# Kernel optimization log

Hardware: AMD Instinct MI355X
Metric: run time of the kernel (lower is better)

Reference implementation:

```python
import jax, jax.numpy as jnp
import numpy as np
import math

DIM = 512
BLOCK_NUM = 16
SEQ_LEN = 8192
BLOCK_LEN = SEQ_LEN // BLOCK_NUM  # 512 == DIM -> mask used as-is
BATCH = 4
LN_EPS = 1e-3  # keras LayerNormalization default epsilon


def setup_inputs() -> dict:
    key = jax.random.key(0)
    ks = jax.random.split(key, 5)
    inputs = jax.random.normal(ks[0], (BATCH, BLOCK_NUM, BLOCK_LEN, DIM), dtype=jnp.float32)
    # binary padding-style mask, values in {0,1}
    mask_array = jax.random.randint(ks[1], (BATCH, SEQ_LEN, DIM), 0, 2).astype(jnp.float32)
    scale = 1.0 / math.sqrt(DIM)
    dw1 = jax.random.normal(ks[2], (DIM, DIM), dtype=jnp.float32) * scale
    dw2 = jax.random.normal(ks[3], (DIM, DIM), dtype=jnp.float32) * scale
    dw3 = jax.random.normal(ks[4], (DIM, DIM), dtype=jnp.float32) * scale
    db1 = jnp.zeros((DIM,), dtype=jnp.float32)
    db2 = jnp.zeros((DIM,), dtype=jnp.float32)
    db3 = jnp.zeros((DIM,), dtype=jnp.float32)
    return {"inputs": inputs, "mask_array": mask_array,
            "dw1": dw1, "dw2": dw2, "dw3": dw3,
            "db1": db1, "db2": db2, "db3": db3}


def reference(inputs, mask_array, dw1, dw2, dw3, db1, db2, db3):
    # inputs: [B, block_num, block_len, dim]
    Q = jnp.matmul(inputs, dw1) + db1
    K = jnp.matmul(inputs, dw2) + db2
    V = jnpp_matmul = jnp.matmul(inputs, dw3) + db3
    V = jnp.matmul(inputs, dw3) + db3
    # block-local attention scores: [B, bn, bl, bl]
    scores = jnp.einsum('bnqd,bnkd->bnqk', Q, K) / math.sqrt(DIM)
    # mask: [B, seq_len, dim] -> [B, bn, bl, dim]; block_len == dim so no slice/tile
    m = mask_array.reshape(BATCH, BLOCK_NUM, BLOCK_LEN, DIM)
    scores = scores + (1.0 - m) * jnp.float32(-1e10)
    p = jax.nn.softmax(scores, axis=-1)
    out = jnp.einsum('bnqk,bnkd->bnqd', p, V) + inputs  # residual
    # LayerNorm(axis=-1), fresh keras layer: gamma=1, beta=0, eps=1e-3
    mean = jnp.mean(out, axis=-1, keepdims=True)
    var = jnp.mean(jnp.square(out - mean), axis=-1, keepdims=True)
    return (out - mean) / jnp.sqrt(var + LN_EPS)
```

## Files before the change

### kernel.cpp

```cpp
#include <hip/hip_runtime.h>

#define DIMK 512
#define NBLK 64
#define NTOK 32768

typedef short  short8 __attribute__((ext_vector_type(8)));
typedef float  f32x4  __attribute__((ext_vector_type(4)));
typedef unsigned short u16x8 __attribute__((ext_vector_type(8)));

__device__ __forceinline__ unsigned short f2bf(float f) {
  union { float f; unsigned u; } v; v.f = f;
  unsigned r = (v.u + 0x7FFFu + ((v.u >> 16) & 1u)) >> 16;
  return (unsigned short)r;
}
__device__ __forceinline__ float bf2f(unsigned short h) {
  return __uint_as_float(((unsigned)h) << 16);
}

__device__ __forceinline__ void gload_lds16(const unsigned short* g,
                                            unsigned short* l) {
  __builtin_amdgcn_global_load_lds(
      (const __attribute__((address_space(1))) unsigned int*)(g),
      (__attribute__((address_space(3))) unsigned int*)(l),
      16, 0, 0);
}

__global__ __launch_bounds__(256) void k_wt_prep(
    const float* __restrict__ dw1, const float* __restrict__ dw2,
    const float* __restrict__ dw3, unsigned short* __restrict__ Wt)
{
  const int idx = blockIdx.x * 256 + threadIdx.x;
  const int w = idx >> 18;
  const int r = idx & 262143;
  const int n = r >> 9, k = r & 511;
  const float* dw = (w == 0) ? dw1 : (w == 1) ? dw2 : dw3;
  Wt[(size_t)w * 262144 + (size_t)n * 512 + k] = f2bf(dw[(size_t)k * 512 + n]);
}

__global__ __launch_bounds__(256) void k_xconv(
    const float* __restrict__ X, unsigned short* __restrict__ Xb)
{
  const size_t i = ((size_t)blockIdx.x * 256 + threadIdx.x) * 8;
  const float4 a = *(const float4*)(X + i);
  const float4 b = *(const float4*)(X + i + 4);
  u16x8 o;
  o[0] = f2bf(a.x); o[1] = f2bf(a.y); o[2] = f2bf(a.z); o[3] = f2bf(a.w);
  o[4] = f2bf(b.x); o[5] = f2bf(b.y); o[6] = f2bf(b.z); o[7] = f2bf(b.w);
  *(u16x8*)(Xb + i) = o;
}

__global__ __launch_bounds__(256) void k_bitpack(
    const float* __restrict__ mask, unsigned char* __restrict__ bits)
{
  const size_t gid = (size_t)blockIdx.x * 256 + threadIdx.x;
  const size_t i = gid * 8;
  const float4 ma = *(const float4*)(mask + i);
  const float4 mb = *(const float4*)(mask + i + 4);
  unsigned v = 0;
  v |= (ma.x > 0.5f) << 0; v |= (ma.y > 0.5f) << 1;
  v |= (ma.z > 0.5f) << 2; v |= (ma.w > 0.5f) << 3;
  v |= (mb.x > 0.5f) << 4; v |= (mb.y > 0.5f) << 5;
  v |= (mb.z > 0.5f) << 6; v |= (mb.w > 0.5f) << 7;
  bits[gid] = (unsigned char)v;
}

__global__ __launch_bounds__(256, 2) void k_qkv(
    const unsigned short* __restrict__ Xb, const unsigned short* __restrict__ Wt,
    const float* __restrict__ db1, const float* __restrict__ db2,
    const float* __restrict__ db3,
    unsigned short* __restrict__ Qb, unsigned short* __restrict__ Kb,
    unsigned short* __restrict__ Vt)
{
  __shared__ __align__(16) unsigned short smem[128 * 136];
  unsigned short* As = smem;
  unsigned short* Bs = smem + 4096;

  const int id = blockIdx.x;
  const int x = id & 7, j = id >> 3;
  const int mtile = x * 32 + (j >> 2);
  const int nt = j & 3;
  const size_t m0 = (size_t)mtile * 128;
  const int n0 = nt * 128;

  const int tid = threadIdx.x, lane = tid & 63, wv = tid >> 6;
  const int quad = lane >> 4, l16 = lane & 15;
  const int rb = (wv >> 1) * 64, cb = (wv & 1) * 64;

  f32x4 acc[3][4][4];
#pragma unroll
  for (int w = 0; w < 3; ++w)
#pragma unroll
    for (int i = 0; i < 4; ++i)
#pragma unroll
      for (int jj = 0; jj < 4; ++jj) {
        f32x4 z = {0.f, 0.f, 0.f, 0.f}; acc[w][i][jj] = z;
      }

  const int ra0 = tid >> 2,          oa0 = (tid & 3) << 3;
  const int ra1 = (tid + 256) >> 2,  oa1 = ((tid + 256) & 3) << 3;
  const unsigned short* a0 = &Xb[(m0 + ra0) * (size_t)DIMK + oa0];
  const unsigned short* a1 = &Xb[(m0 + ra1) * (size_t)DIMK + oa1];

  for (int it = 0; it < 16; ++it) {
    const int k0 = it * 32;
    gload_lds16(a0 + k0, &As[tid * 8]);
    gload_lds16(a1 + k0, &As[(tid + 256) * 8]);
#pragma unroll
    for (int h = 0; h < 6; ++h) {
      const int c = tid + h * 256;
      const int w = c >> 9, cc = c & 511;
      const int r = cc >> 2, o = (cc & 3) << 3;
      gload_lds16(&Wt[(size_t)w * 262144 + (size_t)(n0 + r) * 512 + k0 + o],
                  &Bs[w * 4096 + cc * 8]);
    }
    __syncthreads();
    short8 af[4];
#pragma unroll
    for (int i = 0; i < 4; ++i)
      af[i] = *(const short8*)&As[(rb + i * 16 + l16) * 32 + quad * 8];
#pragma unroll
    for (int jj = 0; jj < 4; ++jj)
#pragma unroll
      for (int w = 0; w < 3; ++w) {
        const short8 bf =
            *(const short8*)&Bs[w * 4096 + (cb + jj * 16 + l16) * 32 + quad * 8];
#pragma unroll
        for (int i = 0; i < 4; ++i)
          acc[w][i][jj] = __builtin_amdgcn_mfma_f32_16x16x32_bf16(
              af[i], bf, acc[w][i][jj], 0, 0, 0);
      }
    __syncthreads();
  }

#pragma unroll
  for (int w = 0; w < 2; ++w) {
    const float* db = (w == 0) ? db1 : db2;
    unsigned short* Ob = (w == 0) ? Qb : Kb;
#pragma unroll
    for (int i = 0; i < 4; ++i)
#pragma unroll
      for (int jj = 0; jj < 4; ++jj)
#pragma unroll
        for (int r = 0; r < 4; ++r) {
          const size_t row = m0 + rb + i * 16 + quad * 4 + r;
          const int col = n0 + cb + jj * 16 + l16;
          Ob[row * (size_t)DIMK + col] = f2bf(acc[w][i][jj][r] + db[col]);
        }
  }
#pragma unroll
  for (int i = 0; i < 4; ++i)
#pragma unroll
    for (int jj = 0; jj < 4; ++jj) {
      const int cl = cb + jj * 16 + l16;
      const int t0 = rb + i * 16 + quad * 4;
      const float bv = db3[n0 + cl];
      ushort4 pk;
      pk.x = f2bf(acc[2][i][jj][0] + bv);
      pk.y = f2bf(acc[2][i][jj][1] + bv);
      pk.z = f2bf(acc[2][i][jj][2] + bv);
      pk.w = f2bf(acc[2][i][jj][3] + bv);
      *(ushort4*)&smem[cl * 136 + t0] = pk;
    }
  __syncthreads();
  const int blk = mtile >> 2;
  const int tokbase = (mtile & 3) * 128;
  unsigned short* Vblk = Vt + (size_t)blk * 262144;
#pragma unroll
  for (int h = 0; h < 8; ++h) {
    const int c = tid + h * 256;
    const int cl = c >> 4, toff = (c & 15) * 8;
    *(u16x8*)&Vblk[(size_t)(n0 + cl) * 512 + tokbase + toff] =
        *(const u16x8*)&smem[cl * 136 + toff];
  }
}

__global__ __launch_bounds__(256, 2) void k_attn_p(
    const unsigned short* __restrict__ Qb, const unsigned short* __restrict__ Kb,
    const unsigned long long* __restrict__ bits, unsigned short* __restrict__ Pb)
{
  __shared__ __align__(16) unsigned short As[64 * 32];
  __shared__ __align__(16) unsigned short Bs[512 * 32];
  __shared__ float red[4][64];
  const int tid = threadIdx.x, lane = tid & 63, wv = tid >> 6;
  const int quad = lane >> 4, l16 = lane & 15;
  const int blk = blockIdx.x & 63, mt = blockIdx.x >> 6;
  const size_t tb = (size_t)blk * 512;
  const size_t q0 = tb + (size_t)mt * 64;

  f32x4 acc[4][8];
#pragma unroll
  for (int i = 0; i < 4; ++i)
#pragma unroll
    for (int j = 0; j < 8; ++j) { f32x4 z = {0.f, 0.f, 0.f, 0.f}; acc[i][j] = z; }

  const int ra = tid >> 2, oa = (tid & 3) << 3;
  const unsigned short* ap = &Qb[(q0 + ra) * (size_t)DIMK + oa];
  const unsigned short* kp = &Kb[tb * (size_t)DIMK];

  for (int it = 0; it < 16; ++it) {
    const int k0 = it * 32;
    gload_lds16(ap + k0, &As[tid * 8]);
#pragma unroll
    for (int h = 0; h < 8; ++h) {
      const int c = tid + h * 256;
      const int r = c >> 2, o = (c & 3) << 3;
      gload_lds16(kp + (size_t)r * DIMK + k0 + o, &Bs[c * 8]);
    }
    __syncthreads();
    short8 af[4], bfv[8];
#pragma unroll
    for (int i = 0; i < 4; ++i)
      af[i] = *(const short8*)&As[(i * 16 + l16) * 32 + quad * 8];
#pragma unroll
    for (int j = 0; j < 8; ++j)
      bfv[j] = *(const short8*)&Bs[(wv * 128 + j * 16 + l16) * 32 + quad * 8];
#pragma unroll
    for (int i = 0; i < 4; ++i)
#pragma unroll
      for (int j = 0; j < 8; ++j)
        acc[i][j] = __builtin_amdgcn_mfma_f32_16x16x32_bf16(
            af[i], bfv[j], acc[i][j], 0, 0, 0);
    __syncthreads();
  }

  const float scale = 0.04419417382415922f;
  float rmax[4][4];
#pragma unroll
  for (int i = 0; i < 4; ++i)
#pragma unroll
    for (int r = 0; r < 4; ++r) rmax[i][r] = -3.0e38f;
#pragma unroll
  for (int i = 0; i < 4; ++i)
#pragma unroll
    for (int r = 0; r < 4; ++r) {
      const size_t tok = q0 + i * 16 + quad * 4 + r;
      const unsigned long long w0 = bits[tok * 8 + wv * 2];
      const unsigned long long w1 = bits[tok * 8 + wv * 2 + 1];
#pragma unroll
      for (int j = 0; j < 8; ++j) {
        const unsigned long long sel = (j < 4) ? w0 : w1;
        const float bias = ((sel >> (l16 + 16 * (j & 3))) & 1ull) ? 0.0f : -1e10f;
        const float v = acc[i][j][r] * scale + bias;
        acc[i][j][r] = v;
        rmax[i][r] = fmaxf(rmax[i][r], v);
      }
    }
#pragma unroll
  for (int i = 0; i < 4; ++i)
#pragma unroll
    for (int r = 0; r < 4; ++r)
      for (int d = 1; d < 16; d <<= 1)
        rmax[i][r] = fmaxf(rmax[i][r], __shfl_xor(rmax[i][r], d, 64));
  if (l16 == 0)
#pragma unroll
    for (int i = 0; i < 4; ++i)
#pragma unroll
      for (int r = 0; r < 4; ++r) red[wv][i * 16 + quad * 4 + r] = rmax[i][r];
  __syncthreads();
#pragma unroll
  for (int i = 0; i < 4; ++i)
#pragma unroll
    for (int r = 0; r < 4; ++r) {
      const int row = i * 16 + quad * 4 + r;
      rmax[i][r] = fmaxf(fmaxf(red[0][row], red[1][row]),
                         fmaxf(red[2][row], red[3][row]));
    }
  __syncthreads();
  float rsum[4][4];
#pragma unroll
  for (int i = 0; i < 4; ++i)
#pragma unroll
    for (int r = 0; r < 4; ++r) rsum[i][r] = 0.f;
#pragma unroll
  for (int i = 0; i < 4; ++i)
#pragma unroll
    for (int j = 0; j < 8; ++j)
#pragma unroll
      for (int r = 0; r < 4; ++r) {
        const float e = __expf(acc[i][j][r] - rmax[i][r]);
        acc[i][j][r] = e;
        rsum[i][r] += e;
      }
#pragma unroll
  for (int i = 0; i < 4; ++i)
#pragma unroll
    for (int r = 0; r < 4; ++r)
      for (int d = 1; d < 16; d <<= 1)
        rsum[i][r] += __shfl_xor(rsum[i][r], d, 64);
  if (l16 == 0)
#pragma unroll
    for (int i = 0; i < 4; ++i)
#pragma unroll
      for (int r = 0; r < 4; ++r) red[wv][i * 16 + quad * 4 + r] = rsum[i][r];
  __syncthreads();
#pragma unroll
  for (int i = 0; i < 4; ++i)
#pragma unroll
    for (int r = 0; r < 4; ++r) {
      const int row = i * 16 + quad * 4 + r;
      rsum[i][r] = 1.0f / (red[0][row] + red[1][row] + red[2][row] + red[3][row]);
    }
#pragma unroll
  for (int i = 0; i < 4; ++i)
#pragma unroll
    for (int j = 0; j < 8; ++j)
#pragma unroll
      for (int r = 0; r < 4; ++r) {
        const size_t tok = q0 + i * 16 + quad * 4 + r;
        const int col = wv * 128 + j * 16 + l16;
        Pb[tok * (size_t)DIMK + col] = f2bf(acc[i][j][r] * rsum[i][r]);
      }
}

__global__ __launch_bounds__(256, 2) void k_pv_ln(
    const unsigned short* __restrict__ Pb, const unsigned short* __restrict__ Vt,
    const unsigned short* __restrict__ Xb, float* __restrict__ Out)
{
  __shared__ __align__(16) unsigned short As[64 * 32];
  __shared__ __align__(16) unsigned short Bs[512 * 32];
  __shared__ float2 red[4][64];
  const int tid = threadIdx.x, lane = tid & 63, wv = tid >> 6;
  const int quad = lane >> 4, l16 = lane & 15;
  const int blk = blockIdx.x & 63, mt = blockIdx.x >> 6;
  const size_t tb = (size_t)blk * 512;
  const size_t q0 = tb + (size_t)mt * 64;

  f32x4 acc[4][8];
#pragma unroll
  for (int i = 0; i < 4; ++i)
#pragma unroll
    for (int j = 0; j < 8; ++j) { f32x4 z = {0.f, 0.f, 0.f, 0.f}; acc[i][j] = z; }

  const int ra = tid >> 2, oa = (tid & 3) << 3;
  const unsigned short* ap = &Pb[(q0 + ra) * (size_t)DIMK + oa];
  const unsigned short* vp = Vt + (size_t)blk * 262144;

  for (int it = 0; it < 16; ++it) {
    const int k0 = it * 32;
    gload_lds16(ap + k0, &As[tid * 8]);
#pragma unroll
    for (int h = 0; h < 8; ++h) {
      const int c = tid + h * 256;
      const int r = c >> 2, o = (c & 3) << 3;
      gload_lds16(vp + (size_t)r * DIMK + k0 + o, &Bs[c * 8]);
    }
    __syncthreads();
    short8 af[4], bfv[8];
#pragma unroll
    for (int i = 0; i < 4; ++i)
      af[i] = *(const short8*)&As[(i * 16 + l16) * 32 + quad * 8];
#pragma unroll
    for (int j = 0; j < 8; ++j)
      bfv[j] = *(const short8*)&Bs[(wv * 128 + j * 16 + l16) * 32 + quad * 8];
#pragma unroll
    for (int i = 0; i < 4; ++i)
#pragma unroll
      for (int j = 0; j < 8; ++j)
        acc[i][j] = __builtin_amdgcn_mfma_f32_16x16x32_bf16(
            af[i], bfv[j], acc[i][j], 0, 0, 0);
    __syncthreads();
  }

  float vsum[4][4], vsq[4][4];
#pragma unroll
  for (int i = 0; i < 4; ++i)
#pragma unroll
    for (int r = 0; r < 4; ++r) { vsum[i][r] = 0.f; vsq[i][r] = 0.f; }
#pragma unroll
  for (int i = 0; i < 4; ++i)
#pragma unroll
    for (int j = 0; j < 8; ++j)
#pragma unroll
      for (int r = 0; r < 4; ++r) {
        const size_t tok = q0 + i * 16 + quad * 4 + r;
        const int col = wv * 128 + j * 16 + l16;
        const float v = acc[i][j][r] + bf2f(Xb[tok * (size_t)DIMK + col]);
        acc[i][j][r] = v;
        vsum[i][r] += v;
        vsq[i][r] += v * v;
      }
#pragma unroll
  for (int i = 0; i < 4; ++i)
#pragma unroll
    for (int r = 0; r < 4; ++r)
      for (int d = 1; d < 16; d <<= 1) {
        vsum[i][r] += __shfl_xor(vsum[i][r], d, 64);
        vsq[i][r]  += __shfl_xor(vsq[i][r], d, 64);
      }
  if (l16 == 0)
#pragma unroll
    for (int i = 0; i < 4; ++i)
#pragma unroll
      for (int r = 0; r < 4; ++r) {
        float2 p; p.x = vsum[i][r]; p.y = vsq[i][r];
        red[wv][i * 16 + quad * 4 + r] = p;
      }
  __syncthreads();
#pragma unroll
  for (int i = 0; i < 4; ++i)
#pragma unroll
    for (int r = 0; r < 4; ++r) {
      const int row = i * 16 + quad * 4 + r;
      float s = 0.f, q = 0.f;
#pragma unroll
      for (int w = 0; w < 4; ++w) { s += red[w][row].x; q += red[w][row].y; }
      const float mean = s * (1.0f / 512.0f);
      const float var  = q * (1.0f / 512.0f) - mean * mean;
      vsum[i][r] = mean;
      vsq[i][r]  = rsqrtf(var + 1e-3f);
    }
#pragma unroll
  for (int i = 0; i < 4; ++i)
#pragma unroll
    for (int j = 0; j < 8; ++j)
#pragma unroll
      for (int r = 0; r < 4; ++r) {
        const size_t tok = q0 + i * 16 + quad * 4 + r;
        const int col = wv * 128 + j * 16 + l16;
        Out[tok * (size_t)DIMK + col] =
            (acc[i][j][r] - vsum[i][r]) * vsq[i][r];
      }
}

extern "C" void kernel_launch(void* const* d_in, const int* in_sizes, int n_in,
                              void* d_out, int out_size, void* d_ws, size_t ws_size,
                              hipStream_t stream)
{
  const float* X    = (const float*)d_in[0];
  const float* mask = (const float*)d_in[1];
  const float* dw1  = (const float*)d_in[2];
  const float* dw2  = (const float*)d_in[3];
  const float* dw3  = (const float*)d_in[4];
  const float* db1  = (const float*)d_in[5];
  const float* db2  = (const float*)d_in[6];
  const float* db3  = (const float*)d_in[7];
  float* Out = (float*)d_out;

  char* ws = (char*)d_ws;
  const size_t MB = 1ull << 20;
  unsigned short* Wt = (unsigned short*)(ws);
  unsigned short* Qb = (unsigned short*)(ws + 2 * MB);
  unsigned short* Kb = (unsigned short*)(ws + 34 * MB);
  unsigned short* Vt = (unsigned short*)(ws + 66 * MB);
  unsigned short* Xb = (unsigned short*)(ws + 98 * MB);
  unsigned short* Pb = Qb;
  unsigned char*  bits = (unsigned char*)d_out;

  k_wt_prep<<<3072, 256, 0, stream>>>(dw1, dw2, dw3, Wt);
  k_xconv  <<<8192, 256, 0, stream>>>(X, Xb);
  k_bitpack<<<8192, 256, 0, stream>>>(mask, bits);
  k_qkv    <<<1024, 256, 0, stream>>>(Xb, Wt, db1, db2, db3, Qb, Kb, Vt);
  k_attn_p <<<512, 256, 0, stream>>>(Qb, Kb, (const unsigned long long*)bits, Pb);
  k_pv_ln  <<<512, 256, 0, stream>>>(Pb, Vt, Xb, Out);
}
```

Before: 344.5 us.

## Fuse softmax and PV/LayerNorm kernels, read mask directly, merge prep kernels

Merges the X and weight bf16 conversion kernels into one launch and drops the mask bitpack kernel. The attention kernel now reads the float mask directly during the score epilogue. It keeps the normalized P tile in LDS instead of writing it to global memory, and runs the PV matmul plus LayerNorm in the same kernel. The QKV kernel's V-transpose staging is split into two passes over a smaller LDS buffer, with launch bounds raised to 4 blocks. Costs: the fused attention kernel uses about 100KB of LDS at 1 block per CU, and it reads the full fp32 mask (256MB... actually 512MB of traffic is avoided only partially) instead of packed bits, though the bitpack kernel no longer has to read it.

Measured after the change: 860.7 us. 150% more time.

```diff
diff --git a/kernel.cpp b/kernel.cpp
--- a/kernel.cpp
+++ b/kernel.cpp
@@ -25,53 +25,38 @@
       16, 0, 0);
 }
 
-__global__ __launch_bounds__(256) void k_wt_prep(
-    const float* __restrict__ dw1, const float* __restrict__ dw2,
-    const float* __restrict__ dw3, unsigned short* __restrict__ Wt)
+__global__ __launch_bounds__(256) void k_prep(
+    const float* __restrict__ X, const float* __restrict__ dw1,
+    const float* __restrict__ dw2, const float* __restrict__ dw3,
+    unsigned short* __restrict__ Xb, unsigned short* __restrict__ Wt)
 {
-  const int idx = blockIdx.x * 256 + threadIdx.x;
-  const int w = idx >> 18;
-  const int r = idx & 262143;
-  const int n = r >> 9, k = r & 511;
-  const float* dw = (w == 0) ? dw1 : (w == 1) ? dw2 : dw3;
-  Wt[(size_t)w * 262144 + (size_t)n * 512 + k] = f2bf(dw[(size_t)k * 512 + n]);
-}
-
-__global__ __launch_bounds__(256) void k_xconv(
-    const float* __restrict__ X, unsigned short* __restrict__ Xb)
-{
-  const size_t i = ((size_t)blockIdx.x * 256 + threadIdx.x) * 8;
-  const float4 a = *(const float4*)(X + i);
-  const float4 b = *(const float4*)(X + i + 4);
-  u16x8 o;
-  o[0] = f2bf(a.x); o[1] = f2bf(a.y); o[2] = f2bf(a.z); o[3] = f2bf(a.w);
-  o[4] = f2bf(b.x); o[5] = f2bf(b.y); o[6] = f2bf(b.z); o[7] = f2bf(b.w);
-  *(u16x8*)(Xb + i) = o;
-}
-
-__global__ __launch_bounds__(256) void k_bitpack(
-    const float* __restrict__ mask, unsigned char* __restrict__ bits)
-{
-  const size_t gid = (size_t)blockIdx.x * 256 + threadIdx.x;
-  const size_t i = gid * 8;
-  const float4 ma = *(const float4*)(mask + i);
-  const float4 mb = *(const float4*)(mask + i + 4);
-  unsigned v = 0;
-  v |= (ma.x > 0.5f) << 0; v |= (ma.y > 0.5f) << 1;
-  v |= (ma.z > 0.5f) << 2; v |= (ma.w > 0.5f) << 3;
-  v |= (mb.x > 0.5f) << 4; v |= (mb.y > 0.5f) << 5;
-  v |= (mb.z > 0.5f) << 6; v |= (mb.w > 0.5f) << 7;
-  bits[gid] = (unsigned char)v;
-}
-
-__global__ __launch_bounds__(256, 2) void k_qkv(
+  const int id = blockIdx.x;
+  if (id < 8192) {
+    const size_t i = ((size_t)id * 256 + threadIdx.x) * 8;
+    const float4 a = *(const float4*)(X + i);
+    const float4 b = *(const float4*)(X + i + 4);
+    u16x8 o;
+    o[0] = f2bf(a.x); o[1] = f2bf(a.y); o[2] = f2bf(a.z); o[3] = f2bf(a.w);
+    o[4] = f2bf(b.x); o[5] = f2bf(b.y); o[6] = f2bf(b.z); o[7] = f2bf(b.w);
+    *(u16x8*)(Xb + i) = o;
+  } else {
+    const int idx = (id - 8192) * 256 + threadIdx.x;
+    const int w = idx >> 18;
+    const int r = idx & 262143;
+    const int n = r >> 9, k = r & 511;
+    const float* dw = (w == 0) ? dw1 : (w == 1) ? dw2 : dw3;
+    Wt[(size_t)w * 262144 + (size_t)n * 512 + k] = f2bf(dw[(size_t)k * 512 + n]);
+  }
+}
+
+__global__ __launch_bounds__(256, 4) void k_qkv(
     const unsigned short* __restrict__ Xb, const unsigned short* __restrict__ Wt,
     const float* __restrict__ db1, const float* __restrict__ db2,
     const float* __restrict__ db3,
     unsigned short* __restrict__ Qb, unsigned short* __restrict__ Kb,
     unsigned short* __restrict__ Vt)
 {
-  __shared__ __align__(16) unsigned short smem[128 * 136];
+  __shared__ __align__(16) unsigned short smem[16384];
   unsigned short* As = smem;
   unsigned short* Bs = smem + 4096;
 
@@ -147,40 +132,51 @@
           Ob[row * (size_t)DIMK + col] = f2bf(acc[w][i][jj][r] + db[col]);
         }
   }
-#pragma unroll
-  for (int i = 0; i < 4; ++i)
-#pragma unroll
-    for (int jj = 0; jj < 4; ++jj) {
-      const int cl = cb + jj * 16 + l16;
-      const int t0 = rb + i * 16 + quad * 4;
-      const float bv = db3[n0 + cl];
-      ushort4 pk;
-      pk.x = f2bf(acc[2][i][jj][0] + bv);
-      pk.y = f2bf(acc[2][i][jj][1] + bv);
-      pk.z = f2bf(acc[2][i][jj][2] + bv);
-      pk.w = f2bf(acc[2][i][jj][3] + bv);
-      *(ushort4*)&smem[cl * 136 + t0] = pk;
-    }
-  __syncthreads();
+
   const int blk = mtile >> 2;
   const int tokbase = (mtile & 3) * 128;
   unsigned short* Vblk = Vt + (size_t)blk * 262144;
 #pragma unroll
-  for (int h = 0; h < 8; ++h) {
-    const int c = tid + h * 256;
-    const int cl = c >> 4, toff = (c & 15) * 8;
-    *(u16x8*)&Vblk[(size_t)(n0 + cl) * 512 + tokbase + toff] =
-        *(const u16x8*)&smem[cl * 136 + toff];
-  }
-}
-
-__global__ __launch_bounds__(256, 2) void k_attn_p(
+  for (int pass = 0; pass < 2; ++pass) {
+    if (pass) __syncthreads();
+    if ((wv & 1) == pass) {
+#pragma unroll
+      for (int i = 0; i < 4; ++i)
+#pragma unroll
+        for (int jj = 0; jj < 4; ++jj) {
+          const int cl = jj * 16 + l16;
+          const int t0 = rb + i * 16 + quad * 4;
+          const float bv = db3[n0 + pass * 64 + cl];
+          ushort4 pk;
+          pk.x = f2bf(acc[2][i][jj][0] + bv);
+          pk.y = f2bf(acc[2][i][jj][1] + bv);
+          pk.z = f2bf(acc[2][i][jj][2] + bv);
+          pk.w = f2bf(acc[2][i][jj][3] + bv);
+          *(ushort4*)&smem[cl * 136 + t0] = pk;
+        }
+    }
+    __syncthreads();
+#pragma unroll
+    for (int h = 0; h < 4; ++h) {
+      const int c = tid + h * 256;
+      const int cl = c >> 4, toff = (c & 15) * 8;
+      *(u16x8*)&Vblk[(size_t)(n0 + pass * 64 + cl) * 512 + tokbase + toff] =
+          *(const u16x8*)&smem[cl * 136 + toff];
+    }
+  }
+}
+
+__global__ __launch_bounds__(256, 1) void k_attn(
     const unsigned short* __restrict__ Qb, const unsigned short* __restrict__ Kb,
-    const unsigned long long* __restrict__ bits, unsigned short* __restrict__ Pb)
+    const unsigned short* __restrict__ Vt, const float* __restrict__ mask,
+    const unsigned short* __restrict__ Xb, float* __restrict__ Out)
 {
+  __shared__ __align__(16) unsigned short Pl[64 * 520];
   __shared__ __align__(16) unsigned short As[64 * 32];
   __shared__ __align__(16) unsigned short Bs[512 * 32];
-  __shared__ float red[4][64];
+  __shared__ float  redA[4][64];
+  __shared__ float2 redB[4][64];
+
   const int tid = threadIdx.x, lane = tid & 63, wv = tid >> 6;
   const int quad = lane >> 4, l16 = lane & 15;
   const int blk = blockIdx.x & 63, mt = blockIdx.x >> 6;
@@ -232,19 +228,16 @@
 #pragma unroll
   for (int i = 0; i < 4; ++i)
 #pragma unroll
-    for (int r = 0; r < 4; ++r) {
-      const size_t tok = q0 + i * 16 + quad * 4 + r;
-      const unsigned long long w0 = bits[tok * 8 + wv * 2];
-      const unsigned long long w1 = bits[tok * 8 + wv * 2 + 1];
-#pragma unroll
-      for (int j = 0; j < 8; ++j) {
-        const unsigned long long sel = (j < 4) ? w0 : w1;
-        const float bias = ((sel >> (l16 + 16 * (j & 3))) & 1ull) ? 0.0f : -1e10f;
-        const float v = acc[i][j][r] * scale + bias;
+    for (int j = 0; j < 8; ++j)
+#pragma unroll
+      for (int r = 0; r < 4; ++r) {
+        const size_t tok = q0 + i * 16 + quad * 4 + r;
+        const int col = wv * 128 + j * 16 + l16;
+        const float m = mask[tok * (size_t)DIMK + col];
+        const float v = acc[i][j][r] * scale + (1.0f - m) * (-1e10f);
         acc[i][j][r] = v;
         rmax[i][r] = fmaxf(rmax[i][r], v);
       }
-    }
 #pragma unroll
   for (int i = 0; i < 4; ++i)
 #pragma unroll
@@ -255,15 +248,15 @@
 #pragma unroll
     for (int i = 0; i < 4; ++i)
 #pragma unroll
-      for (int r = 0; r < 4; ++r) red[wv][i * 16 + quad * 4 + r] = rmax[i][r];
+      for (int r = 0; r < 4; ++r) redA[wv][i * 16 + quad * 4 + r] = rmax[i][r];
   __syncthreads();
 #pragma unroll
   for (int i = 0; i < 4; ++i)
 #pragma unroll
     for (int r = 0; r < 4; ++r) {
       const int row = i * 16 + quad * 4 + r;
-      rmax[i][r] = fmaxf(fmaxf(red[0][row], red[1][row]),
-                         fmaxf(red[2][row], red[3][row]));
+      rmax[i][r] = fmaxf(fmaxf(redA[0][row], redA[1][row]),
+                         fmaxf(redA[2][row], redA[3][row]));
     }
   __syncthreads();
   float rsum[4][4];
@@ -291,53 +284,36 @@
 #pragma unroll
     for (int i = 0; i < 4; ++i)
 #pragma unroll
-      for (int r = 0; r < 4; ++r) red[wv][i * 16 + quad * 4 + r] = rsum[i][r];
+      for (int r = 0; r < 4; ++r) redA[wv][i * 16 + quad * 4 + r] = rsum[i][r];
   __syncthreads();
 #pragma unroll
   for (int i = 0; i < 4; ++i)
 #pragma unroll
     for (int r = 0; r < 4; ++r) {
       const int row = i * 16 + quad * 4 + r;
-      rsum[i][r] = 1.0f / (red[0][row] + red[1][row] + red[2][row] + red[3][row]);
-    }
-#pragma unroll
-  for (int i = 0; i < 4; ++i)
-#pragma unroll
-    for (int j = 0; j < 8; ++j)
-#pragma unroll
-      for (int r = 0; r < 4; ++r) {
-        const size_t tok = q0 + i * 16 + quad * 4 + r;
-        const int col = wv * 128 + j * 16 + l16;
-        Pb[tok * (size_t)DIMK + col] = f2bf(acc[i][j][r] * rsum[i][r]);
-      }
-}
-
-__global__ __launch_bounds__(256, 2) void k_pv_ln(
-    const unsigned short* __restrict__ Pb, const unsigned short* __restrict__ Vt,
-    const unsigned short* __restrict__ Xb, float* __restrict__ Out)
-{
-  __shared__ __align__(16) unsigned short As[64 * 32];
-  __shared__ __align__(16) unsigned short Bs[512 * 32];
-  __shared__ float2 red[4][64];
-  const int tid = threadIdx.x, lane = tid & 63, wv = tid >> 6;
-  const int quad = lane >> 4, l16 = lane & 15;
-  const int blk = blockIdx.x & 63, mt = blockIdx.x >> 6;
-  const size_t tb = (size_t)blk * 512;
-  const size_t q0 = tb + (size_t)mt * 64;
-
-  f32x4 acc[4][8];
+      rsum[i][r] = 1.0f / (redA[0][row] + redA[1][row] +
+                           redA[2][row] + redA[3][row]);
+    }
+#pragma unroll
+  for (int i = 0; i < 4; ++i)
+#pragma unroll
+    for (int j = 0; j < 8; ++j)
+#pragma unroll
+      for (int r = 0; r < 4; ++r) {
+        const int q = i * 16 + quad * 4 + r;
+        const int key = wv * 128 + j * 16 + l16;
+        Pl[q * 520 + key] = f2bf(acc[i][j][r] * rsum[i][r]);
+      }
+  __syncthreads();
+
 #pragma unroll
   for (int i = 0; i < 4; ++i)
 #pragma unroll
     for (int j = 0; j < 8; ++j) { f32x4 z = {0.f, 0.f, 0.f, 0.f}; acc[i][j] = z; }
 
-  const int ra = tid >> 2, oa = (tid & 3) << 3;
-  const unsigned short* ap = &Pb[(q0 + ra) * (size_t)DIMK + oa];
   const unsigned short* vp = Vt + (size_t)blk * 262144;
-
   for (int it = 0; it < 16; ++it) {
     const int k0 = it * 32;
-    gload_lds16(ap + k0, &As[tid * 8]);
 #pragma unroll
     for (int h = 0; h < 8; ++h) {
       const int c = tid + h * 256;
@@ -348,7 +324,7 @@
     short8 af[4], bfv[8];
 #pragma unroll
     for (int i = 0; i < 4; ++i)
-      af[i] = *(const short8*)&As[(i * 16 + l16) * 32 + quad * 8];
+      af[i] = *(const short8*)&Pl[(i * 16 + l16) * 520 + k0 + quad * 8];
 #pragma unroll
     for (int j = 0; j < 8; ++j)
       bfv[j] = *(const short8*)&Bs[(wv * 128 + j * 16 + l16) * 32 + quad * 8];
@@ -393,7 +369,7 @@
 #pragma unroll
       for (int r = 0; r < 4; ++r) {
         float2 p; p.x = vsum[i][r]; p.y = vsq[i][r];
-        red[wv][i * 16 + quad * 4 + r] = p;
+        redB[wv][i * 16 + quad * 4 + r] = p;
       }
   __syncthreads();
 #pragma unroll
@@ -403,7 +379,7 @@
       const int row = i * 16 + quad * 4 + r;
       float s = 0.f, q = 0.f;
 #pragma unroll
-      for (int w = 0; w < 4; ++w) { s += red[w][row].x; q += red[w][row].y; }
+      for (int w = 0; w < 4; ++w) { s += redB[w][row].x; q += redB[w][row].y; }
       const float mean = s * (1.0f / 512.0f);
       const float var  = q * (1.0f / 512.0f) - mean * mean;
       vsum[i][r] = mean;
@@ -443,13 +419,8 @@
   unsigned short* Kb = (unsigned short*)(ws + 34 * MB);
   unsigned short* Vt = (unsigned short*)(ws + 66 * MB);
   unsigned short* Xb = (unsigned short*)(ws + 98 * MB);
-  unsigned short* Pb = Qb;
-  unsigned char*  bits = (unsigned char*)d_out;
-
-  k_wt_prep<<<3072, 256, 0, stream>>>(dw1, dw2, dw3, Wt);
-  k_xconv  <<<8192, 256, 0, stream>>>(X, Xb);
-  k_bitpack<<<8192, 256, 0, stream>>>(mask, bits);
-  k_qkv    <<<1024, 256, 0, stream>>>(Xb, Wt, db1, db2, db3, Qb, Kb, Vt);
-  k_attn_p <<<512, 256, 0, stream>>>(Qb, Kb, (const unsigned long long*)bits, Pb);
-  k_pv_ln  <<<512, 256, 0, stream>>>(Pb, Vt, Xb, Out);
-}
+
+  k_prep<<<11264, 256, 0, stream>>>(X, dw1, dw2, dw3, Xb, Wt);
+  k_qkv <<<1024, 256, 0, stream>>>(Xb, Wt, db1, db2, db3, Qb, Kb, Vt);
+  k_attn<<<512, 256, 0, stream>>>(Qb, Kb, Vt, mask, Xb, Out);
+}
```
